# Performance work log

Measured on AMD Instinct MI355X. Metric: run time of the kernel, lower is better.

## Reference

```python
import jax, jax.numpy as jnp
import numpy as np

NEAR, FAR, N_SAMPLES = 0.5, 2.5, 64


def setup_inputs() -> dict:
    key = jax.random.key(0)
    ks = jax.random.split(key, 12)
    N = 4096
    W = 256  # MLP width
    inp = {
        "rays_o": jax.random.normal(ks[0], (N, 3), jnp.float32),
        "rays_d": jax.random.normal(ks[1], (N, 3), jnp.float32),
        "t_rand": jax.random.uniform(ks[2], (N, N_SAMPLES), jnp.float32),
        "W1": jax.random.normal(ks[3], (3, W), jnp.float32) * 0.5,
        "b1": jnp.zeros((W,), jnp.float32),
        "W2": jax.random.normal(ks[4], (W, W), jnp.float32) * (1.0 / np.sqrt(W)),
        "b2": jnp.zeros((W,), jnp.float32),
        "W3": jax.random.normal(ks[5], (W, W), jnp.float32) * (1.0 / np.sqrt(W)),
        "b3": jnp.zeros((W,), jnp.float32),
        "Wd": jax.random.normal(ks[6], (W, 1), jnp.float32) * (1.0 / np.sqrt(W)),
        "bd": jnp.zeros((1,), jnp.float32),
        "W4": jax.random.normal(ks[7], (W + 3, 128), jnp.float32) * (1.0 / np.sqrt(W + 3)),
        "b4": jnp.zeros((128,), jnp.float32),
        "W5": jax.random.normal(ks[8], (128, 3), jnp.float32) * (1.0 / np.sqrt(128)),
        "b5": jnp.zeros((3,), jnp.float32),
    }
    return inp


def _nerf_mlp(pts, viewdirs, W1, b1, W2, b2, W3, b3, Wd, bd, W4, b4, W5, b5):
    # pts, viewdirs: [N, S, 3] -> rgb [N, S, 3], density [N, S]
    h = jax.nn.relu(pts @ W1 + b1)
    h = jax.nn.relu(h @ W2 + b2)
    h = jax.nn.relu(h @ W3 + b3)
    density = (h @ Wd + bd)[..., 0]
    h2 = jax.nn.relu(jnp.concatenate([h, viewdirs], axis=-1) @ W4 + b4)
    rgb = jax.nn.sigmoid(h2 @ W5 + b5)
    return rgb, density


def reference(rays_o, rays_d, t_rand, W1, b1, W2, b2, W3, b3, Wd, bd, W4, b4, W5, b5):
    N = rays_o.shape[0]
    # Stratified sampling along rays
    t_vals = jnp.linspace(0.0, 1.0, N_SAMPLES, dtype=jnp.float32)
    z = NEAR * (1.0 - t_vals) + FAR * t_vals                      # [S]
    z_vals = jnp.broadcast_to(z, (N, N_SAMPLES))
    mids = 0.5 * (z_vals[:, 1:] + z_vals[:, :-1])
    upper = jnp.concatenate([mids, z_vals[:, -1:]], axis=-1)
    lower = jnp.concatenate([z_vals[:, :1], mids], axis=-1)
    z_vals = lower + (upper - lower) * t_rand                      # [N, S]

    pts = rays_o[:, None, :] + rays_d[:, None, :] * z_vals[..., None]  # [N, S, 3]
    viewdirs = rays_d / (jnp.linalg.norm(rays_d, axis=-1, keepdims=True) + 1e-8)
    vdirs = jnp.broadcast_to(viewdirs[:, None, :], pts.shape)

    rgb, density = _nerf_mlp(pts, vdirs, W1, b1, W2, b2, W3, b3, Wd, bd, W4, b4, W5, b5)

    # Alpha compositing
    dists = z_vals[:, 1:] - z_vals[:, :-1]
    dists = jnp.concatenate([dists, jnp.full_like(dists[:, :1], 1e10)], axis=-1)
    alpha = 1.0 - jnp.exp(-jax.nn.relu(density) * dists)           # [N, S]
    trans = jnp.cumprod(
        jnp.concatenate([jnp.ones_like(alpha[:, :1]), 1.0 - alpha[:, :-1] + 1e-10], axis=-1),
        axis=-1,
    )
    weights = alpha * trans                                        # [N, S]
    rgb_map = jnp.sum(weights[..., None] * rgb, axis=-2)           # [N, 3]
    depth_map = jnp.sum(weights * z_vals, axis=-1)                 # [N]
    acc_map = jnp.sum(weights, axis=-1)                            # [N]
    rgb_map = rgb_map + (1.0 - acc_map[..., None])  # white background
    return rgb_map, depth_map, acc_map
```

## Files before the change

### kernel.cpp

```cpp
#include <hip/hip_runtime.h>
#include <stdint.h>


#define NRAYS 4096

typedef unsigned short u16;
typedef __attribute__((ext_vector_type(8))) short short8;
typedef __attribute__((ext_vector_type(4))) float f32x4;

__device__ __forceinline__ u16 f2bf(float f) {
  union { float f; uint32_t i; } v; v.f = f;
  return (u16)((v.i + 0x7FFFu + ((v.i >> 16) & 1u)) >> 16);
}
__device__ __forceinline__ float bf2f(u16 u) {
  union { uint32_t i; float f; } v; v.i = ((uint32_t)u) << 16; return v.f;
}
__device__ __forceinline__ uint32_t cvtpk(float lo, float hi) {
  uint32_t r;
  asm("v_cvt_pk_bf16_f32 %0, %1, %2" : "=v"(r) : "v"(lo), "v"(hi));
  return r;
}

__device__ __forceinline__ float zval(int j, float tr) {
  float fj = (float)j;
  float zj = 0.5f + 2.0f * (fj / 63.0f);
  float lower = (j == 0)  ? zj : 0.5f * (zj + (0.5f + 2.0f * ((fj - 1.0f) / 63.0f)));
  float upper = (j == 63) ? zj : 0.5f * (zj + (0.5f + 2.0f * ((fj + 1.0f) / 63.0f)));
  return lower + (upper - lower) * tr;
}

__device__ __forceinline__ int fragidx(int n, int k) {
  return ((((n >> 4) * 8 + (k >> 5)) * 64 + ((k >> 3) & 3) * 16 + (n & 15)) << 3) + (k & 7);
}
__device__ __forceinline__ int fragidx32(int n, int k) {
  return (((n >> 4) * 64 + ((k >> 3) & 3) * 16 + (n & 15)) << 3) + (k & 7);
}

__global__ void pack_weights(const float* __restrict__ W1, const float* __restrict__ b1,
                             const float* __restrict__ W2, const float* __restrict__ W3,
                             const float* __restrict__ W4, const float* __restrict__ Wd,
                             const float* __restrict__ W5, u16* __restrict__ ws) {
  int idx = blockIdx.x * 256 + threadIdx.x;
  float v;
  int dst;
  if (idx < 65536) {
    int k = idx >> 8, n = idx & 255;
    v = W2[idx];
    dst = fragidx(n, k);
  } else if (idx < 131072) {
    int o = idx - 65536, k = o >> 8, n = o & 255;
    v = W3[o];
    dst = 65536 + fragidx(n, k);
  } else if (idx < 163840) {
    int o = idx - 131072, k = o >> 7, n = o & 127;
    v = W4[o];
    dst = 131072 + fragidx(n, k);
  } else if (idx < 167936) {
    int o = idx - 163840, k = o >> 4, n = o & 15;
    v = (n == 0) ? Wd[k] : 0.f;
    dst = 163840 + fragidx(n, k);
  } else if (idx < 169984) {
    int o = idx - 167936, k = o >> 4, n = o & 15;
    v = (n < 3) ? W5[k * 3 + n] : 0.f;
    dst = 167936 + fragidx(n, k);
  } else {
    int o = idx - 169984, k = o >> 8, n = o & 255;
    if (k < 6)      v = W1[(k >> 1) * 256 + n];
    else if (k == 6) v = b1[n];
    else            v = 0.f;
    dst = 169984 + fragidx32(n, k);
  }
  ws[dst] = f2bf(v);
}

#define MFMA __builtin_amdgcn_mfma_f32_16x16x32_bf16
#define ZER4 (f32x4){0.f, 0.f, 0.f, 0.f}

#define LDA4(ACT, SQ)                                                          \
    short8 av0 = *(const short8*)((ACT) + m0 * 256 + (((SQ) ^ (m0 & 31)) << 3)); \
    short8 av1 = *(const short8*)((ACT) + m1 * 256 + (((SQ) ^ (m1 & 31)) << 3)); \
    short8 av2 = *(const short8*)((ACT) + m2 * 256 + (((SQ) ^ (m2 & 31)) << 3)); \
    short8 av3 = *(const short8*)((ACT) + m3 * 256 + (((SQ) ^ (m3 & 31)) << 3))

#define MF16v(B0, B1, B2_, B3_) do {                                         \
    c00 = MFMA(av0, B0, c00, 0, 0, 0); c10 = MFMA(av1, B0, c10, 0, 0, 0);    \
    c20 = MFMA(av2, B0, c20, 0, 0, 0); c30 = MFMA(av3, B0, c30, 0, 0, 0);    \
    c01 = MFMA(av0, B1, c01, 0, 0, 0); c11 = MFMA(av1, B1, c11, 0, 0, 0);    \
    c21 = MFMA(av2, B1, c21, 0, 0, 0); c31 = MFMA(av3, B1, c31, 0, 0, 0);    \
    c02 = MFMA(av0, B2_, c02, 0, 0, 0); c12 = MFMA(av1, B2_, c12, 0, 0, 0);  \
    c22 = MFMA(av2, B2_, c22, 0, 0, 0); c32 = MFMA(av3, B2_, c32, 0, 0, 0);  \
    c03 = MFMA(av0, B3_, c03, 0, 0, 0); c13 = MFMA(av1, B3_, c13, 0, 0, 0);  \
    c23 = MFMA(av2, B3_, c23, 0, 0, 0); c33 = MFMA(av3, B3_, c33, 0, 0, 0);  \
  } while (0)

#define EPIC(CV, mt, ng, addv, ACT) do {                                     \
    int su_ = ((ng) >> 3), so_ = ((ng) & 7);                                 \
    float f0_ = fmaxf((CV)[0] + (addv), 0.f);                                \
    float f1_ = fmaxf((CV)[1] + (addv), 0.f);                                \
    float f2_ = fmaxf((CV)[2] + (addv), 0.f);                                \
    float f3_ = fmaxf((CV)[3] + (addv), 0.f);                                \
    uint32_t p01_ = cvtpk(f0_, f1_), p23_ = cvtpk(f2_, f3_);                 \
    int mmb_ = (mt) * 16 + quad * 4;                                         \
    (ACT)[(mmb_ + 0) * 256 + ((su_ ^ ((mmb_ + 0) & 31)) << 3) + so_] = (u16)p01_;         \
    (ACT)[(mmb_ + 1) * 256 + ((su_ ^ ((mmb_ + 1) & 31)) << 3) + so_] = (u16)(p01_ >> 16); \
    (ACT)[(mmb_ + 2) * 256 + ((su_ ^ ((mmb_ + 2) & 31)) << 3) + so_] = (u16)p23_;         \
    (ACT)[(mmb_ + 3) * 256 + ((su_ ^ ((mmb_ + 3) & 31)) << 3) + so_] = (u16)(p23_ >> 16); \
  } while (0)

__global__ void __launch_bounds__(256, 2) nerf_fused(
    const float* __restrict__ rays_o, const float* __restrict__ rays_d,
    const float* __restrict__ t_rand,
    const float* __restrict__ b2, const float* __restrict__ b3,
    const float* __restrict__ bd,
    const float* __restrict__ W4, const float* __restrict__ b4,
    const float* __restrict__ b5,
    const u16* __restrict__ wpack, float* __restrict__ out) {
  __shared__ u16   actA[64 * 256];
  __shared__ u16   actB[64 * 256];
  __shared__ float dens[64];
  __shared__ float rgbL[64 * 4];

  const int t = threadIdx.x;
  const int lane = t & 63;
  const int wv = t >> 6;
  const int quad = lane >> 4;
  const int l15 = lane & 15;
  const int ray = blockIdx.x;
  const int m0 = l15, m1 = l15 + 16, m2 = l15 + 32, m3 = l15 + 48;

  short8 W1f0, W1f1, W1f2, W1f3;
  {
    const u16* w1b = wpack + 169984 + (wv * 4) * 512 + lane * 8;
    W1f0 = *(const short8*)(w1b);
    W1f1 = *(const short8*)(w1b + 512);
    W1f2 = *(const short8*)(w1b + 1024);
    W1f3 = *(const short8*)(w1b + 1536);
  }
  short8 B2a[8], B2b[8], B2c[8], B2d[8];
  const u16* q0 = wpack + (wv * 4 + 0) * 4096 + lane * 8;
  const u16* q1 = wpack + (wv * 4 + 1) * 4096 + lane * 8;
  const u16* q2 = wpack + (wv * 4 + 2) * 4096 + lane * 8;
  const u16* q3 = wpack + (wv * 4 + 3) * 4096 + lane * 8;
#pragma unroll
  for (int kq = 0; kq < 4; kq++) {
    B2a[kq] = *(const short8*)(q0 + kq * 512);
    B2b[kq] = *(const short8*)(q1 + kq * 512);
    B2c[kq] = *(const short8*)(q2 + kq * 512);
    B2d[kq] = *(const short8*)(q3 + kq * 512);
  }

  const float rox = rays_o[ray * 3 + 0], roy = rays_o[ray * 3 + 1], roz = rays_o[ray * 3 + 2];
  const float rdx = rays_d[ray * 3 + 0], rdy = rays_d[ray * 3 + 1], rdz = rays_d[ray * 3 + 2];

  {
    short8 avz = {0, 0, 0, 0, 0, 0, 0, 0};
    short8 av0 = avz, av1 = avz, av2 = avz, av3 = avz;
    if (quad == 0) {
#pragma unroll
      for (int r = 0; r < 4; r++) {
        int m = l15 + r * 16;
        float tr = t_rand[ray * 64 + m];
        float zm = zval(m, tr);
        float px = rox + rdx * zm, py = roy + rdy * zm, pz = roz + rdz * zm;
        u16 xh = f2bf(px); float xl = px - bf2f(xh);
        u16 yh = f2bf(py); float yl = py - bf2f(yh);
        u16 zh = f2bf(pz); float zl = pz - bf2f(zh);
        short8 f;
        f[0] = (short)xh; f[1] = (short)f2bf(xl);
        f[2] = (short)yh; f[3] = (short)f2bf(yl);
        f[4] = (short)zh; f[5] = (short)f2bf(zl);
        f[6] = (short)0x3F80; f[7] = 0;
        if (r == 0) av0 = f; else if (r == 1) av1 = f;
        else if (r == 2) av2 = f; else av3 = f;
      }
    }
    f32x4 c00 = ZER4, c01 = ZER4, c02 = ZER4, c03 = ZER4;
    f32x4 c10 = ZER4, c11 = ZER4, c12 = ZER4, c13 = ZER4;
    f32x4 c20 = ZER4, c21 = ZER4, c22 = ZER4, c23 = ZER4;
    f32x4 c30 = ZER4, c31 = ZER4, c32 = ZER4, c33 = ZER4;
    MF16v(W1f0, W1f1, W1f2, W1f3);
    int ng0 = wv * 64 + l15;
    EPIC(c00, 0, ng0, 0.f, actA); EPIC(c10, 1, ng0, 0.f, actA);
    EPIC(c20, 2, ng0, 0.f, actA); EPIC(c30, 3, ng0, 0.f, actA);
    EPIC(c01, 0, ng0 + 16, 0.f, actA); EPIC(c11, 1, ng0 + 16, 0.f, actA);
    EPIC(c21, 2, ng0 + 16, 0.f, actA); EPIC(c31, 3, ng0 + 16, 0.f, actA);
    EPIC(c02, 0, ng0 + 32, 0.f, actA); EPIC(c12, 1, ng0 + 32, 0.f, actA);
    EPIC(c22, 2, ng0 + 32, 0.f, actA); EPIC(c32, 3, ng0 + 32, 0.f, actA);
    EPIC(c03, 0, ng0 + 48, 0.f, actA); EPIC(c13, 1, ng0 + 48, 0.f, actA);
    EPIC(c23, 2, ng0 + 48, 0.f, actA); EPIC(c33, 3, ng0 + 48, 0.f, actA);
  }
#pragma unroll
  for (int kq = 4; kq < 8; kq++) {
    B2a[kq] = *(const short8*)(q0 + kq * 512);
    B2b[kq] = *(const short8*)(q1 + kq * 512);
    B2c[kq] = *(const short8*)(q2 + kq * 512);
    B2d[kq] = *(const short8*)(q3 + kq * 512);
  }
  __syncthreads();

  short8 B3a[4], B3b[4], B3c[4], B3d[4];

  {
    int ng0 = wv * 64 + l15;
    float bi0 = b2[ng0], bi1 = b2[ng0 + 16], bi2 = b2[ng0 + 32], bi3 = b2[ng0 + 48];
    f32x4 c00 = ZER4, c01 = ZER4, c02 = ZER4, c03 = ZER4;
    f32x4 c10 = ZER4, c11 = ZER4, c12 = ZER4, c13 = ZER4;
    f32x4 c20 = ZER4, c21 = ZER4, c22 = ZER4, c23 = ZER4;
    f32x4 c30 = ZER4, c31 = ZER4, c32 = ZER4, c33 = ZER4;
#pragma unroll
    for (int kq = 0; kq < 8; kq++) {
      LDA4(actA, kq * 4 + quad);
      MF16v(B2a[kq], B2b[kq], B2c[kq], B2d[kq]);
    }
    {
      const u16* r0 = wpack + 65536 + (wv * 4 + 0) * 4096 + lane * 8;
      const u16* r1 = wpack + 65536 + (wv * 4 + 1) * 4096 + lane * 8;
      const u16* r2 = wpack + 65536 + (wv * 4 + 2) * 4096 + lane * 8;
      const u16* r3 = wpack + 65536 + (wv * 4 + 3) * 4096 + lane * 8;
#pragma unroll
      for (int kq = 0; kq < 4; kq++) {
        B3a[kq] = *(const short8*)(r0 + kq * 512);
        B3b[kq] = *(const short8*)(r1 + kq * 512);
        B3c[kq] = *(const short8*)(r2 + kq * 512);
        B3d[kq] = *(const short8*)(r3 + kq * 512);
      }
    }
    EPIC(c00, 0, ng0, bi0, actB); EPIC(c10, 1, ng0, bi0, actB);
    EPIC(c20, 2, ng0, bi0, actB); EPIC(c30, 3, ng0, bi0, actB);
    EPIC(c01, 0, ng0 + 16, bi1, actB); EPIC(c11, 1, ng0 + 16, bi1, actB);
    EPIC(c21, 2, ng0 + 16, bi1, actB); EPIC(c31, 3, ng0 + 16, bi1, actB);
    EPIC(c02, 0, ng0 + 32, bi2, actB); EPIC(c12, 1, ng0 + 32, bi2, actB);
    EPIC(c22, 2, ng0 + 32, bi2, actB); EPIC(c32, 3, ng0 + 32, bi2, actB);
    EPIC(c03, 0, ng0 + 48, bi3, actB); EPIC(c13, 1, ng0 + 48, bi3, actB);
    EPIC(c23, 2, ng0 + 48, bi3, actB); EPIC(c33, 3, ng0 + 48, bi3, actB);
  }
  __syncthreads();

  short8 L4a[2], L4b[2], L4d[2];

  {
    int ng0 = wv * 64 + l15;
    float bi0 = b3[ng0], bi1 = b3[ng0 + 16], bi2 = b3[ng0 + 32], bi3 = b3[ng0 + 48];
    const u16* r0 = wpack + 65536 + (wv * 4 + 0) * 4096 + lane * 8;
    const u16* r1 = wpack + 65536 + (wv * 4 + 1) * 4096 + lane * 8;
    const u16* r2 = wpack + 65536 + (wv * 4 + 2) * 4096 + lane * 8;
    const u16* r3 = wpack + 65536 + (wv * 4 + 3) * 4096 + lane * 8;
    f32x4 c00 = ZER4, c01 = ZER4, c02 = ZER4, c03 = ZER4;
    f32x4 c10 = ZER4, c11 = ZER4, c12 = ZER4, c13 = ZER4;
    f32x4 c20 = ZER4, c21 = ZER4, c22 = ZER4, c23 = ZER4;
    f32x4 c30 = ZER4, c31 = ZER4, c32 = ZER4, c33 = ZER4;
#pragma unroll
    for (int kq = 0; kq < 8; kq++) {
      short8 b0, b1v, b2v, b3v;
      if (kq < 4) { b0 = B3a[kq]; b1v = B3b[kq]; b2v = B3c[kq]; b3v = B3d[kq]; }
      else {
        b0 = *(const short8*)(r0 + kq * 512);
        b1v = *(const short8*)(r1 + kq * 512);
        b2v = *(const short8*)(r2 + kq * 512);
        b3v = *(const short8*)(r3 + kq * 512);
      }
      LDA4(actB, kq * 4 + quad);
      MF16v(b0, b1v, b2v, b3v);
    }
    {
      const u16* s0 = wpack + 131072 + (wv * 2 + 0) * 4096 + lane * 8;
      const u16* s1 = wpack + 131072 + (wv * 2 + 1) * 4096 + lane * 8;
      const u16* sD = wpack + 163840 + lane * 8;
#pragma unroll
      for (int kq = 0; kq < 2; kq++) {
        L4a[kq] = *(const short8*)(s0 + kq * 512);
        L4b[kq] = *(const short8*)(s1 + kq * 512);
        L4d[kq] = *(const short8*)(sD + kq * 512);
      }
    }
    EPIC(c00, 0, ng0, bi0, actA); EPIC(c10, 1, ng0, bi0, actA);
    EPIC(c20, 2, ng0, bi0, actA); EPIC(c30, 3, ng0, bi0, actA);
    EPIC(c01, 0, ng0 + 16, bi1, actA); EPIC(c11, 1, ng0 + 16, bi1, actA);
    EPIC(c21, 2, ng0 + 16, bi1, actA); EPIC(c31, 3, ng0 + 16, bi1, actA);
    EPIC(c02, 0, ng0 + 32, bi2, actA); EPIC(c12, 1, ng0 + 32, bi2, actA);
    EPIC(c22, 2, ng0 + 32, bi2, actA); EPIC(c32, 3, ng0 + 32, bi2, actA);
    EPIC(c03, 0, ng0 + 48, bi3, actA); EPIC(c13, 1, ng0 + 48, bi3, actA);
    EPIC(c23, 2, ng0 + 48, bi3, actA); EPIC(c33, 3, ng0 + 48, bi3, actA);
  }
  __syncthreads();

  short8 W5f[4];

  {
    float nrm = sqrtf(rdx * rdx + rdy * rdy + rdz * rdz) + 1e-8f;
    float v0 = rdx / nrm, v1 = rdy / nrm, v2 = rdz / nrm;
    int ng0 = wv * 32 + l15;
    int ng1 = ng0 + 16;
    float ad0 = b4[ng0] + v0 * W4[32768 + ng0] + v1 * W4[32896 + ng0] + v2 * W4[33024 + ng0];
    float ad1 = b4[ng1] + v0 * W4[32768 + ng1] + v1 * W4[32896 + ng1] + v2 * W4[33024 + ng1];
    const u16* s0 = wpack + 131072 + (wv * 2 + 0) * 4096 + lane * 8;
    const u16* s1 = wpack + 131072 + (wv * 2 + 1) * 4096 + lane * 8;
    const u16* sD = wpack + 163840 + lane * 8;
    f32x4 c00 = ZER4, c01 = ZER4;
    f32x4 c10 = ZER4, c11 = ZER4;
    f32x4 c20 = ZER4, c21 = ZER4;
    f32x4 c30 = ZER4, c31 = ZER4;
    f32x4 c40 = ZER4, c41 = ZER4, c42 = ZER4, c43 = ZER4;
#pragma unroll
    for (int kq = 0; kq < 8; kq++) {
      short8 b0 = (kq < 2) ? L4a[kq] : *(const short8*)(s0 + kq * 512);
      short8 b1v = (kq < 2) ? L4b[kq] : *(const short8*)(s1 + kq * 512);
      short8 bD = (kq < 2) ? L4d[kq] : *(const short8*)(sD + kq * 512);
      LDA4(actA, kq * 4 + quad);
      c00 = MFMA(av0, b0, c00, 0, 0, 0); c10 = MFMA(av1, b0, c10, 0, 0, 0);
      c20 = MFMA(av2, b0, c20, 0, 0, 0); c30 = MFMA(av3, b0, c30, 0, 0, 0);
      c01 = MFMA(av0, b1v, c01, 0, 0, 0); c11 = MFMA(av1, b1v, c11, 0, 0, 0);
      c21 = MFMA(av2, b1v, c21, 0, 0, 0); c31 = MFMA(av3, b1v, c31, 0, 0, 0);
      c40 = MFMA(av0, bD, c40, 0, 0, 0); c41 = MFMA(av1, bD, c41, 0, 0, 0);
      c42 = MFMA(av2, bD, c42, 0, 0, 0); c43 = MFMA(av3, bD, c43, 0, 0, 0);
    }
    if (wv == 0) {
      const u16* s5 = wpack + 167936 + lane * 8;
#pragma unroll
      for (int kq = 0; kq < 4; kq++) W5f[kq] = *(const short8*)(s5 + kq * 512);
    }
    EPIC(c00, 0, ng0, ad0, actB); EPIC(c10, 1, ng0, ad0, actB);
    EPIC(c20, 2, ng0, ad0, actB); EPIC(c30, 3, ng0, ad0, actB);
    EPIC(c01, 0, ng1, ad1, actB); EPIC(c11, 1, ng1, ad1, actB);
    EPIC(c21, 2, ng1, ad1, actB); EPIC(c31, 3, ng1, ad1, actB);
    if (wv == 0 && l15 == 0) {
#pragma unroll
      for (int r = 0; r < 4; r++) {
        dens[ 0 + quad * 4 + r] = c40[r];
        dens[16 + quad * 4 + r] = c41[r];
        dens[32 + quad * 4 + r] = c42[r];
        dens[48 + quad * 4 + r] = c43[r];
      }
    }
  }
  __syncthreads();

  if (wv == 0) {
    {
      f32x4 cR0 = ZER4, cR1 = ZER4, cR2 = ZER4, cR3 = ZER4;
#pragma unroll
      for (int kq = 0; kq < 4; kq++) {
        LDA4(actB, kq * 4 + quad);
        cR0 = MFMA(av0, W5f[kq], cR0, 0, 0, 0);
        cR1 = MFMA(av1, W5f[kq], cR1, 0, 0, 0);
        cR2 = MFMA(av2, W5f[kq], cR2, 0, 0, 0);
        cR3 = MFMA(av3, W5f[kq], cR3, 0, 0, 0);
      }
      if (l15 < 3) {
        float b5v = b5[l15];
#pragma unroll
        for (int r = 0; r < 4; r++) {
          rgbL[( 0 + quad * 4 + r) * 4 + l15] = 1.f / (1.f + __expf(-(cR0[r] + b5v)));
          rgbL[(16 + quad * 4 + r) * 4 + l15] = 1.f / (1.f + __expf(-(cR1[r] + b5v)));
          rgbL[(32 + quad * 4 + r) * 4 + l15] = 1.f / (1.f + __expf(-(cR2[r] + b5v)));
          rgbL[(48 + quad * 4 + r) * 4 + l15] = 1.f / (1.f + __expf(-(cR3[r] + b5v)));
        }
      }
    }
    {
      int j = lane;
      float tr = t_rand[ray * 64 + j];
      float zvj = zval(j, tr);
      float zvn = __shfl_down(zvj, 1);
      float dist = (j < 63) ? (zvn - zvj) : 1e10f;
      float bd0 = bd[0];
      float alpha = 1.f - __expf(-fmaxf(dens[j] + bd0, 0.f) * dist);
      float v = 1.f - alpha + 1e-10f;
      float pscan = v;
#pragma unroll
      for (int d = 1; d < 64; d <<= 1) {
        float o = __shfl_up(pscan, d);
        if (j >= d) pscan *= o;
      }
      float T = __shfl_up(pscan, 1);
      if (j == 0) T = 1.f;
      float w = alpha * T;
      float r0 = w * rgbL[j * 4 + 0];
      float r1 = w * rgbL[j * 4 + 1];
      float r2 = w * rgbL[j * 4 + 2];
      float dp = w * zvj;
      float ac = w;
#pragma unroll
      for (int d = 32; d; d >>= 1) {
        r0 += __shfl_down(r0, d);
        r1 += __shfl_down(r1, d);
        r2 += __shfl_down(r2, d);
        dp += __shfl_down(dp, d);
        ac += __shfl_down(ac, d);
      }
      if (j == 0) {
        float bg = 1.f - ac;
        out[ray * 3 + 0] = r0 + bg;
        out[ray * 3 + 1] = r1 + bg;
        out[ray * 3 + 2] = r2 + bg;
        out[NRAYS * 3 + ray] = dp;
        out[NRAYS * 4 + ray] = ac;
      }
    }
  }
}

extern "C" void kernel_launch(void* const* d_in, const int* in_sizes, int n_in,
                              void* d_out, int out_size, void* d_ws, size_t ws_size,
                              hipStream_t stream) {
  const float* rays_o = (const float*)d_in[0];
  const float* rays_d = (const float*)d_in[1];
  const float* t_rand = (const float*)d_in[2];
  const float* W1 = (const float*)d_in[3];
  const float* b1 = (const float*)d_in[4];
  const float* W2 = (const float*)d_in[5];
  const float* b2 = (const float*)d_in[6];
  const float* W3 = (const float*)d_in[7];
  const float* b3 = (const float*)d_in[8];
  const float* Wd = (const float*)d_in[9];
  const float* bd = (const float*)d_in[10];
  const float* W4 = (const float*)d_in[11];
  const float* b4 = (const float*)d_in[12];
  const float* W5 = (const float*)d_in[13];
  const float* b5 = (const float*)d_in[14];
  u16* wpack = (u16*)d_ws;
  float* out = (float*)d_out;

  pack_weights<<<696, 256, 0, stream>>>(W1, b1, W2, W3, W4, Wd, W5, wpack);
  nerf_fused<<<NRAYS, 256, 0, stream>>>(rays_o, rays_d, t_rand, b2, b3,
                                        bd, W4, b4, b5, wpack, out);
}
```

Measured before the change: 232.7 us.

## Stream weights with double-buffered registers, shrink LDS, raise occupancy to 3 blocks

Replaces the full per-layer register arrays of weight fragments with two rolling buffers of B fragments, prefetched one k-chunk ahead inside a non-unrolled loop. The two 64x256 activation buffers become one in-place buffer, protected by an extra barrier before the epilogue overwrites it, plus a smaller 64x128 buffer for the layer-4 output. Launch bounds go from 2 to 3 blocks per CU. The goal is to cut VGPR and LDS use so more blocks fit per CU, at the cost of less prefetch depth, loop overhead and more barriers.

```diff
diff --git a/kernel.cpp b/kernel.cpp
--- a/kernel.cpp
+++ b/kernel.cpp
@@ -76,11 +76,11 @@
 #define MFMA __builtin_amdgcn_mfma_f32_16x16x32_bf16
 #define ZER4 (f32x4){0.f, 0.f, 0.f, 0.f}
 
-#define LDA4(ACT, SQ)                                                          \
-    short8 av0 = *(const short8*)((ACT) + m0 * 256 + (((SQ) ^ (m0 & 31)) << 3)); \
-    short8 av1 = *(const short8*)((ACT) + m1 * 256 + (((SQ) ^ (m1 & 31)) << 3)); \
-    short8 av2 = *(const short8*)((ACT) + m2 * 256 + (((SQ) ^ (m2 & 31)) << 3)); \
-    short8 av3 = *(const short8*)((ACT) + m3 * 256 + (((SQ) ^ (m3 & 31)) << 3))
+#define LDA4(SQ)                                                               \
+    short8 av0 = *(const short8*)(act + m0 * 256 + (((SQ) ^ (m0 & 31)) << 3)); \
+    short8 av1 = *(const short8*)(act + m1 * 256 + (((SQ) ^ (m1 & 31)) << 3)); \
+    short8 av2 = *(const short8*)(act + m2 * 256 + (((SQ) ^ (m2 & 31)) << 3)); \
+    short8 av3 = *(const short8*)(act + m3 * 256 + (((SQ) ^ (m3 & 31)) << 3))
 
 #define MF16v(B0, B1, B2_, B3_) do {                                         \
     c00 = MFMA(av0, B0, c00, 0, 0, 0); c10 = MFMA(av1, B0, c10, 0, 0, 0);    \
@@ -93,7 +93,16 @@
     c23 = MFMA(av2, B3_, c23, 0, 0, 0); c33 = MFMA(av3, B3_, c33, 0, 0, 0);  \
   } while (0)
 
-#define EPIC(CV, mt, ng, addv, ACT) do {                                     \
+#define MF12v(B0, B1, BD) do {                                               \
+    c00 = MFMA(av0, B0, c00, 0, 0, 0); c10 = MFMA(av1, B0, c10, 0, 0, 0);    \
+    c20 = MFMA(av2, B0, c20, 0, 0, 0); c30 = MFMA(av3, B0, c30, 0, 0, 0);    \
+    c01 = MFMA(av0, B1, c01, 0, 0, 0); c11 = MFMA(av1, B1, c11, 0, 0, 0);    \
+    c21 = MFMA(av2, B1, c21, 0, 0, 0); c31 = MFMA(av3, B1, c31, 0, 0, 0);    \
+    c40 = MFMA(av0, BD, c40, 0, 0, 0); c41 = MFMA(av1, BD, c41, 0, 0, 0);    \
+    c42 = MFMA(av2, BD, c42, 0, 0, 0); c43 = MFMA(av3, BD, c43, 0, 0, 0);    \
+  } while (0)
+
+#define EPIC(CV, mt, ng, addv) do {                                          \
     int su_ = ((ng) >> 3), so_ = ((ng) & 7);                                 \
     float f0_ = fmaxf((CV)[0] + (addv), 0.f);                                \
     float f1_ = fmaxf((CV)[1] + (addv), 0.f);                                \
@@ -101,13 +110,33 @@
     float f3_ = fmaxf((CV)[3] + (addv), 0.f);                                \
     uint32_t p01_ = cvtpk(f0_, f1_), p23_ = cvtpk(f2_, f3_);                 \
     int mmb_ = (mt) * 16 + quad * 4;                                         \
-    (ACT)[(mmb_ + 0) * 256 + ((su_ ^ ((mmb_ + 0) & 31)) << 3) + so_] = (u16)p01_;         \
-    (ACT)[(mmb_ + 1) * 256 + ((su_ ^ ((mmb_ + 1) & 31)) << 3) + so_] = (u16)(p01_ >> 16); \
-    (ACT)[(mmb_ + 2) * 256 + ((su_ ^ ((mmb_ + 2) & 31)) << 3) + so_] = (u16)p23_;         \
-    (ACT)[(mmb_ + 3) * 256 + ((su_ ^ ((mmb_ + 3) & 31)) << 3) + so_] = (u16)(p23_ >> 16); \
+    act[(mmb_ + 0) * 256 + ((su_ ^ ((mmb_ + 0) & 31)) << 3) + so_] = (u16)p01_;         \
+    act[(mmb_ + 1) * 256 + ((su_ ^ ((mmb_ + 1) & 31)) << 3) + so_] = (u16)(p01_ >> 16); \
+    act[(mmb_ + 2) * 256 + ((su_ ^ ((mmb_ + 2) & 31)) << 3) + so_] = (u16)p23_;         \
+    act[(mmb_ + 3) * 256 + ((su_ ^ ((mmb_ + 3) & 31)) << 3) + so_] = (u16)(p23_ >> 16); \
   } while (0)
 
-__global__ void __launch_bounds__(256, 2) nerf_fused(
+#define EPIH(CV, mt, ng, addv) do {                                          \
+    int su_ = ((ng) >> 3), so_ = ((ng) & 7);                                 \
+    float f0_ = fmaxf((CV)[0] + (addv), 0.f);                                \
+    float f1_ = fmaxf((CV)[1] + (addv), 0.f);                                \
+    float f2_ = fmaxf((CV)[2] + (addv), 0.f);                                \
+    float f3_ = fmaxf((CV)[3] + (addv), 0.f);                                \
+    uint32_t p01_ = cvtpk(f0_, f1_), p23_ = cvtpk(f2_, f3_);                 \
+    int mmb_ = (mt) * 16 + quad * 4;                                         \
+    h4L[(mmb_ + 0) * 128 + ((su_ ^ ((mmb_ + 0) & 15)) << 3) + so_] = (u16)p01_;         \
+    h4L[(mmb_ + 1) * 128 + ((su_ ^ ((mmb_ + 1) & 15)) << 3) + so_] = (u16)(p01_ >> 16); \
+    h4L[(mmb_ + 2) * 128 + ((su_ ^ ((mmb_ + 2) & 15)) << 3) + so_] = (u16)p23_;         \
+    h4L[(mmb_ + 3) * 128 + ((su_ ^ ((mmb_ + 3) & 15)) << 3) + so_] = (u16)(p23_ >> 16); \
+  } while (0)
+
+#define LDA4H(SQ)                                                              \
+    short8 av0 = *(const short8*)(h4L + m0 * 128 + (((SQ) ^ (m0 & 15)) << 3)); \
+    short8 av1 = *(const short8*)(h4L + m1 * 128 + (((SQ) ^ (m1 & 15)) << 3)); \
+    short8 av2 = *(const short8*)(h4L + m2 * 128 + (((SQ) ^ (m2 & 15)) << 3)); \
+    short8 av3 = *(const short8*)(h4L + m3 * 128 + (((SQ) ^ (m3 & 15)) << 3))
+
+__global__ void __launch_bounds__(256, 3) nerf_fused(
     const float* __restrict__ rays_o, const float* __restrict__ rays_d,
     const float* __restrict__ t_rand,
     const float* __restrict__ b2, const float* __restrict__ b3,
@@ -115,8 +144,8 @@
     const float* __restrict__ W4, const float* __restrict__ b4,
     const float* __restrict__ b5,
     const u16* __restrict__ wpack, float* __restrict__ out) {
-  __shared__ u16   actA[64 * 256];
-  __shared__ u16   actB[64 * 256];
+  __shared__ u16   act[64 * 256];
+  __shared__ u16   h4L[64 * 128];
   __shared__ float dens[64];
   __shared__ float rgbL[64 * 4];
 
@@ -128,6 +157,8 @@
   const int ray = blockIdx.x;
   const int m0 = l15, m1 = l15 + 16, m2 = l15 + 32, m3 = l15 + 48;
 
+  short8 Pa0, Pa1, Pa2, Pa3, Pb0, Pb1, Pb2, Pb3;
+
   short8 W1f0, W1f1, W1f2, W1f3;
   {
     const u16* w1b = wpack + 169984 + (wv * 4) * 512 + lane * 8;
@@ -136,18 +167,14 @@
     W1f2 = *(const short8*)(w1b + 1024);
     W1f3 = *(const short8*)(w1b + 1536);
   }
-  short8 B2a[8], B2b[8], B2c[8], B2d[8];
   const u16* q0 = wpack + (wv * 4 + 0) * 4096 + lane * 8;
   const u16* q1 = wpack + (wv * 4 + 1) * 4096 + lane * 8;
   const u16* q2 = wpack + (wv * 4 + 2) * 4096 + lane * 8;
   const u16* q3 = wpack + (wv * 4 + 3) * 4096 + lane * 8;
-#pragma unroll
-  for (int kq = 0; kq < 4; kq++) {
-    B2a[kq] = *(const short8*)(q0 + kq * 512);
-    B2b[kq] = *(const short8*)(q1 + kq * 512);
-    B2c[kq] = *(const short8*)(q2 + kq * 512);
-    B2d[kq] = *(const short8*)(q3 + kq * 512);
-  }
+  Pa0 = *(const short8*)(q0);       Pa1 = *(const short8*)(q1);
+  Pa2 = *(const short8*)(q2);       Pa3 = *(const short8*)(q3);
+  Pb0 = *(const short8*)(q0 + 512); Pb1 = *(const short8*)(q1 + 512);
+  Pb2 = *(const short8*)(q2 + 512); Pb3 = *(const short8*)(q3 + 512);
 
   const float rox = rays_o[ray * 3 + 0], roy = rays_o[ray * 3 + 1], roz = rays_o[ray * 3 + 2];
   const float rdx = rays_d[ray * 3 + 0], rdy = rays_d[ray * 3 + 1], rdz = rays_d[ray * 3 + 2];
@@ -180,25 +207,16 @@
     f32x4 c30 = ZER4, c31 = ZER4, c32 = ZER4, c33 = ZER4;
     MF16v(W1f0, W1f1, W1f2, W1f3);
     int ng0 = wv * 64 + l15;
-    EPIC(c00, 0, ng0, 0.f, actA); EPIC(c10, 1, ng0, 0.f, actA);
-    EPIC(c20, 2, ng0, 0.f, actA); EPIC(c30, 3, ng0, 0.f, actA);
-    EPIC(c01, 0, ng0 + 16, 0.f, actA); EPIC(c11, 1, ng0 + 16, 0.f, actA);
-    EPIC(c21, 2, ng0 + 16, 0.f, actA); EPIC(c31, 3, ng0 + 16, 0.f, actA);
-    EPIC(c02, 0, ng0 + 32, 0.f, actA); EPIC(c12, 1, ng0 + 32, 0.f, actA);
-    EPIC(c22, 2, ng0 + 32, 0.f, actA); EPIC(c32, 3, ng0 + 32, 0.f, actA);
-    EPIC(c03, 0, ng0 + 48, 0.f, actA); EPIC(c13, 1, ng0 + 48, 0.f, actA);
-    EPIC(c23, 2, ng0 + 48, 0.f, actA); EPIC(c33, 3, ng0 + 48, 0.f, actA);
-  }
-#pragma unroll
-  for (int kq = 4; kq < 8; kq++) {
-    B2a[kq] = *(const short8*)(q0 + kq * 512);
-    B2b[kq] = *(const short8*)(q1 + kq * 512);
-    B2c[kq] = *(const short8*)(q2 + kq * 512);
-    B2d[kq] = *(const short8*)(q3 + kq * 512);
+    EPIC(c00, 0, ng0, 0.f); EPIC(c10, 1, ng0, 0.f);
+    EPIC(c20, 2, ng0, 0.f); EPIC(c30, 3, ng0, 0.f);
+    EPIC(c01, 0, ng0 + 16, 0.f); EPIC(c11, 1, ng0 + 16, 0.f);
+    EPIC(c21, 2, ng0 + 16, 0.f); EPIC(c31, 3, ng0 + 16, 0.f);
+    EPIC(c02, 0, ng0 + 32, 0.f); EPIC(c12, 1, ng0 + 32, 0.f);
+    EPIC(c22, 2, ng0 + 32, 0.f); EPIC(c32, 3, ng0 + 32, 0.f);
+    EPIC(c03, 0, ng0 + 48, 0.f); EPIC(c13, 1, ng0 + 48, 0.f);
+    EPIC(c23, 2, ng0 + 48, 0.f); EPIC(c33, 3, ng0 + 48, 0.f);
   }
   __syncthreads();
-
-  short8 B3a[4], B3b[4], B3c[4], B3d[4];
 
   {
     int ng0 = wv * 64 + l15;
@@ -207,36 +225,48 @@
     f32x4 c10 = ZER4, c11 = ZER4, c12 = ZER4, c13 = ZER4;
     f32x4 c20 = ZER4, c21 = ZER4, c22 = ZER4, c23 = ZER4;
     f32x4 c30 = ZER4, c31 = ZER4, c32 = ZER4, c33 = ZER4;
-#pragma unroll
-    for (int kq = 0; kq < 8; kq++) {
-      LDA4(actA, kq * 4 + quad);
-      MF16v(B2a[kq], B2b[kq], B2c[kq], B2d[kq]);
-    }
+#pragma unroll 1
+    for (int kc = 0; kc < 3; kc++) {
+      {
+        LDA4((2 * kc) * 4 + quad);
+        MF16v(Pa0, Pa1, Pa2, Pa3);
+      }
+      Pa0 = *(const short8*)(q0 + (2 * kc + 2) * 512);
+      Pa1 = *(const short8*)(q1 + (2 * kc + 2) * 512);
+      Pa2 = *(const short8*)(q2 + (2 * kc + 2) * 512);
+      Pa3 = *(const short8*)(q3 + (2 * kc + 2) * 512);
+      {
+        LDA4((2 * kc + 1) * 4 + quad);
+        MF16v(Pb0, Pb1, Pb2, Pb3);
+      }
+      Pb0 = *(const short8*)(q0 + (2 * kc + 3) * 512);
+      Pb1 = *(const short8*)(q1 + (2 * kc + 3) * 512);
+      Pb2 = *(const short8*)(q2 + (2 * kc + 3) * 512);
+      Pb3 = *(const short8*)(q3 + (2 * kc + 3) * 512);
+    }
+    { LDA4(24 + quad); MF16v(Pa0, Pa1, Pa2, Pa3); }
+    { LDA4(28 + quad); MF16v(Pb0, Pb1, Pb2, Pb3); }
+    __syncthreads();
     {
       const u16* r0 = wpack + 65536 + (wv * 4 + 0) * 4096 + lane * 8;
       const u16* r1 = wpack + 65536 + (wv * 4 + 1) * 4096 + lane * 8;
       const u16* r2 = wpack + 65536 + (wv * 4 + 2) * 4096 + lane * 8;
       const u16* r3 = wpack + 65536 + (wv * 4 + 3) * 4096 + lane * 8;
-#pragma unroll
-      for (int kq = 0; kq < 4; kq++) {
-        B3a[kq] = *(const short8*)(r0 + kq * 512);
-        B3b[kq] = *(const short8*)(r1 + kq * 512);
-        B3c[kq] = *(const short8*)(r2 + kq * 512);
-        B3d[kq] = *(const short8*)(r3 + kq * 512);
-      }
-    }
-    EPIC(c00, 0, ng0, bi0, actB); EPIC(c10, 1, ng0, bi0, actB);
-    EPIC(c20, 2, ng0, bi0, actB); EPIC(c30, 3, ng0, bi0, actB);
-    EPIC(c01, 0, ng0 + 16, bi1, actB); EPIC(c11, 1, ng0 + 16, bi1, actB);
-    EPIC(c21, 2, ng0 + 16, bi1, actB); EPIC(c31, 3, ng0 + 16, bi1, actB);
-    EPIC(c02, 0, ng0 + 32, bi2, actB); EPIC(c12, 1, ng0 + 32, bi2, actB);
-    EPIC(c22, 2, ng0 + 32, bi2, actB); EPIC(c32, 3, ng0 + 32, bi2, actB);
-    EPIC(c03, 0, ng0 + 48, bi3, actB); EPIC(c13, 1, ng0 + 48, bi3, actB);
-    EPIC(c23, 2, ng0 + 48, bi3, actB); EPIC(c33, 3, ng0 + 48, bi3, actB);
+      Pa0 = *(const short8*)(r0);       Pa1 = *(const short8*)(r1);
+      Pa2 = *(const short8*)(r2);       Pa3 = *(const short8*)(r3);
+      Pb0 = *(const short8*)(r0 + 512); Pb1 = *(const short8*)(r1 + 512);
+      Pb2 = *(const short8*)(r2 + 512); Pb3 = *(const short8*)(r3 + 512);
+    }
+    EPIC(c00, 0, ng0, bi0); EPIC(c10, 1, ng0, bi0);
+    EPIC(c20, 2, ng0, bi0); EPIC(c30, 3, ng0, bi0);
+    EPIC(c01, 0, ng0 + 16, bi1); EPIC(c11, 1, ng0 + 16, bi1);
+    EPIC(c21, 2, ng0 + 16, bi1); EPIC(c31, 3, ng0 + 16, bi1);
+    EPIC(c02, 0, ng0 + 32, bi2); EPIC(c12, 1, ng0 + 32, bi2);
+    EPIC(c22, 2, ng0 + 32, bi2); EPIC(c32, 3, ng0 + 32, bi2);
+    EPIC(c03, 0, ng0 + 48, bi3); EPIC(c13, 1, ng0 + 48, bi3);
+    EPIC(c23, 2, ng0 + 48, bi3); EPIC(c33, 3, ng0 + 48, bi3);
   }
   __syncthreads();
-
-  short8 L4a[2], L4b[2], L4d[2];
 
   {
     int ng0 = wv * 64 + l15;
@@ -249,38 +279,45 @@
     f32x4 c10 = ZER4, c11 = ZER4, c12 = ZER4, c13 = ZER4;
     f32x4 c20 = ZER4, c21 = ZER4, c22 = ZER4, c23 = ZER4;
     f32x4 c30 = ZER4, c31 = ZER4, c32 = ZER4, c33 = ZER4;
-#pragma unroll
-    for (int kq = 0; kq < 8; kq++) {
-      short8 b0, b1v, b2v, b3v;
-      if (kq < 4) { b0 = B3a[kq]; b1v = B3b[kq]; b2v = B3c[kq]; b3v = B3d[kq]; }
-      else {
-        b0 = *(const short8*)(r0 + kq * 512);
-        b1v = *(const short8*)(r1 + kq * 512);
-        b2v = *(const short8*)(r2 + kq * 512);
-        b3v = *(const short8*)(r3 + kq * 512);
-      }
-      LDA4(actB, kq * 4 + quad);
-      MF16v(b0, b1v, b2v, b3v);
-    }
+#pragma unroll 1
+    for (int kc = 0; kc < 3; kc++) {
+      {
+        LDA4((2 * kc) * 4 + quad);
+        MF16v(Pa0, Pa1, Pa2, Pa3);
+      }
+      Pa0 = *(const short8*)(r0 + (2 * kc + 2) * 512);
+      Pa1 = *(const short8*)(r1 + (2 * kc + 2) * 512);
+      Pa2 = *(const short8*)(r2 + (2 * kc + 2) * 512);
+      Pa3 = *(const short8*)(r3 + (2 * kc + 2) * 512);
+      {
+        LDA4((2 * kc + 1) * 4 + quad);
+        MF16v(Pb0, Pb1, Pb2, Pb3);
+      }
+      Pb0 = *(const short8*)(r0 + (2 * kc + 3) * 512);
+      Pb1 = *(const short8*)(r1 + (2 * kc + 3) * 512);
+      Pb2 = *(const short8*)(r2 + (2 * kc + 3) * 512);
+      Pb3 = *(const short8*)(r3 + (2 * kc + 3) * 512);
+    }
+    { LDA4(24 + quad); MF16v(Pa0, Pa1, Pa2, Pa3); }
+    { LDA4(28 + quad); MF16v(Pb0, Pb1, Pb2, Pb3); }
+    __syncthreads();
     {
       const u16* s0 = wpack + 131072 + (wv * 2 + 0) * 4096 + lane * 8;
       const u16* s1 = wpack + 131072 + (wv * 2 + 1) * 4096 + lane * 8;
       const u16* sD = wpack + 163840 + lane * 8;
-#pragma unroll
-      for (int kq = 0; kq < 2; kq++) {
-        L4a[kq] = *(const short8*)(s0 + kq * 512);
-        L4b[kq] = *(const short8*)(s1 + kq * 512);
-        L4d[kq] = *(const short8*)(sD + kq * 512);
-      }
-    }
-    EPIC(c00, 0, ng0, bi0, actA); EPIC(c10, 1, ng0, bi0, actA);
-    EPIC(c20, 2, ng0, bi0, actA); EPIC(c30, 3, ng0, bi0, actA);
-    EPIC(c01, 0, ng0 + 16, bi1, actA); EPIC(c11, 1, ng0 + 16, bi1, actA);
-    EPIC(c21, 2, ng0 + 16, bi1, actA); EPIC(c31, 3, ng0 + 16, bi1, actA);
-    EPIC(c02, 0, ng0 + 32, bi2, actA); EPIC(c12, 1, ng0 + 32, bi2, actA);
-    EPIC(c22, 2, ng0 + 32, bi2, actA); EPIC(c32, 3, ng0 + 32, bi2, actA);
-    EPIC(c03, 0, ng0 + 48, bi3, actA); EPIC(c13, 1, ng0 + 48, bi3, actA);
-    EPIC(c23, 2, ng0 + 48, bi3, actA); EPIC(c33, 3, ng0 + 48, bi3, actA);
+      Pa0 = *(const short8*)(s0);       Pa1 = *(const short8*)(s1);
+      Pa2 = *(const short8*)(sD);
+      Pb0 = *(const short8*)(s0 + 512); Pb1 = *(const short8*)(s1 + 512);
+      Pb2 = *(const short8*)(sD + 512);
+    }
+    EPIC(c00, 0, ng0, bi0); EPIC(c10, 1, ng0, bi0);
+    EPIC(c20, 2, ng0, bi0); EPIC(c30, 3, ng0, bi0);
+    EPIC(c01, 0, ng0 + 16, bi1); EPIC(c11, 1, ng0 + 16, bi1);
+    EPIC(c21, 2, ng0 + 16, bi1); EPIC(c31, 3, ng0 + 16, bi1);
+    EPIC(c02, 0, ng0 + 32, bi2); EPIC(c12, 1, ng0 + 32, bi2);
+    EPIC(c22, 2, ng0 + 32, bi2); EPIC(c32, 3, ng0 + 32, bi2);
+    EPIC(c03, 0, ng0 + 48, bi3); EPIC(c13, 1, ng0 + 48, bi3);
+    EPIC(c23, 2, ng0 + 48, bi3); EPIC(c33, 3, ng0 + 48, bi3);
   }
   __syncthreads();
 
@@ -301,28 +338,34 @@
     f32x4 c20 = ZER4, c21 = ZER4;
     f32x4 c30 = ZER4, c31 = ZER4;
     f32x4 c40 = ZER4, c41 = ZER4, c42 = ZER4, c43 = ZER4;
-#pragma unroll
-    for (int kq = 0; kq < 8; kq++) {
-      short8 b0 = (kq < 2) ? L4a[kq] : *(const short8*)(s0 + kq * 512);
-      short8 b1v = (kq < 2) ? L4b[kq] : *(const short8*)(s1 + kq * 512);
-      short8 bD = (kq < 2) ? L4d[kq] : *(const short8*)(sD + kq * 512);
-      LDA4(actA, kq * 4 + quad);
-      c00 = MFMA(av0, b0, c00, 0, 0, 0); c10 = MFMA(av1, b0, c10, 0, 0, 0);
-      c20 = MFMA(av2, b0, c20, 0, 0, 0); c30 = MFMA(av3, b0, c30, 0, 0, 0);
-      c01 = MFMA(av0, b1v, c01, 0, 0, 0); c11 = MFMA(av1, b1v, c11, 0, 0, 0);
-      c21 = MFMA(av2, b1v, c21, 0, 0, 0); c31 = MFMA(av3, b1v, c31, 0, 0, 0);
-      c40 = MFMA(av0, bD, c40, 0, 0, 0); c41 = MFMA(av1, bD, c41, 0, 0, 0);
-      c42 = MFMA(av2, bD, c42, 0, 0, 0); c43 = MFMA(av3, bD, c43, 0, 0, 0);
-    }
+#pragma unroll 1
+    for (int kc = 0; kc < 3; kc++) {
+      {
+        LDA4((2 * kc) * 4 + quad);
+        MF12v(Pa0, Pa1, Pa2);
+      }
+      Pa0 = *(const short8*)(s0 + (2 * kc + 2) * 512);
+      Pa1 = *(const short8*)(s1 + (2 * kc + 2) * 512);
+      Pa2 = *(const short8*)(sD + (2 * kc + 2) * 512);
+      {
+        LDA4((2 * kc + 1) * 4 + quad);
+        MF12v(Pb0, Pb1, Pb2);
+      }
+      Pb0 = *(const short8*)(s0 + (2 * kc + 3) * 512);
+      Pb1 = *(const short8*)(s1 + (2 * kc + 3) * 512);
+      Pb2 = *(const short8*)(sD + (2 * kc + 3) * 512);
+    }
+    { LDA4(24 + quad); MF12v(Pa0, Pa1, Pa2); }
+    { LDA4(28 + quad); MF12v(Pb0, Pb1, Pb2); }
     if (wv == 0) {
       const u16* s5 = wpack + 167936 + lane * 8;
 #pragma unroll
       for (int kq = 0; kq < 4; kq++) W5f[kq] = *(const short8*)(s5 + kq * 512);
     }
-    EPIC(c00, 0, ng0, ad0, actB); EPIC(c10, 1, ng0, ad0, actB);
-    EPIC(c20, 2, ng0, ad0, actB); EPIC(c30, 3, ng0, ad0, actB);
-    EPIC(c01, 0, ng1, ad1, actB); EPIC(c11, 1, ng1, ad1, actB);
-    EPIC(c21, 2, ng1, ad1, actB); EPIC(c31, 3, ng1, ad1, actB);
+    EPIH(c00, 0, ng0, ad0); EPIH(c10, 1, ng0, ad0);
+    EPIH(c20, 2, ng0, ad0); EPIH(c30, 3, ng0, ad0);
+    EPIH(c01, 0, ng1, ad1); EPIH(c11, 1, ng1, ad1);
+    EPIH(c21, 2, ng1, ad1); EPIH(c31, 3, ng1, ad1);
     if (wv == 0 && l15 == 0) {
 #pragma unroll
       for (int r = 0; r < 4; r++) {
@@ -340,7 +383,7 @@
       f32x4 cR0 = ZER4, cR1 = ZER4, cR2 = ZER4, cR3 = ZER4;
 #pragma unroll
       for (int kq = 0; kq < 4; kq++) {
-        LDA4(actB, kq * 4 + quad);
+        LDA4H(kq * 4 + quad);
         cR0 = MFMA(av0, W5f[kq], cR0, 0, 0, 0);
         cR1 = MFMA(av1, W5f[kq], cR1, 0, 0, 0);
         cR2 = MFMA(av2, W5f[kq], cR2, 0, 0, 0);
```

Result: slower. 303.9 us (+30.6%).
